# Performance work log

Measured on AMD Instinct MI355X. Metric: run time of the kernel, lower is better.

Reference implementation:

```python
import jax, jax.numpy as jnp
import numpy as np

HIDDEN = 128
RHO = 5        # K // 2 with K = 10
J = 5
SCALE = 5.0


def setup_inputs() -> dict:
    key = jax.random.key(0)
    ks = jax.random.split(key, 16)
    B, N, D = 2, 4096, HIDDEN
    eigvs = jax.random.uniform(ks[0], (B, N, D), dtype=jnp.float32)  # eigenvalue encodings in [0,1)
    x = jax.random.normal(ks[1], (B, N, D), dtype=jnp.float32)
    U = jax.random.normal(ks[2], (B, N, N), dtype=jnp.float32) / np.sqrt(N)
    s = 1.0 / np.sqrt(D)
    return {
        "eigvs": eigvs, "x": x, "U": U,
        # Linear weights stored as [in, out] (already transposed vs torch)
        "Wa": jax.random.normal(ks[3], (D, RHO), dtype=jnp.float32) * s,
        "ba": jnp.zeros((RHO,), jnp.float32),
        "Wb": jax.random.normal(ks[4], (D, RHO), dtype=jnp.float32) * s,
        "bb": jnp.zeros((RHO,), jnp.float32),
        "Ws": jax.random.normal(ks[5], (D, J), dtype=jnp.float32) * s,
        "bs": jnp.zeros((J,), jnp.float32),
        "WS": jax.random.normal(ks[6], (D, D), dtype=jnp.float32) * s,
        "bS": jnp.zeros((D,), jnp.float32),
        "WM": jax.random.normal(ks[7], (J, D, D), dtype=jnp.float32) * s,
        "bM": jnp.zeros((J, D), jnp.float32),
        "Ww": jax.random.normal(ks[8], (D, D), dtype=jnp.float32) * s,
        "bw": jnp.zeros((D,), jnp.float32),
    }


def _generate_g(a, sx, rho):
    # a: [B, rho]; sx: [B, J, N, D] scaled eigenvalues. Even Chebyshev polys.
    T_odd = jnp.ones_like(sx)
    T_even = sx
    g = a[:, 0, None, None, None] * T_even
    for i in range(1, rho):
        T_odd = 2.0 * sx * T_even - T_odd
        T_even = 2.0 * sx * T_odd - T_even
        g = g + a[:, i, None, None, None] * T_even
    return g


def _generate_h(b, e, rho):
    # b: [B, rho]; e: [B, N, D]. Odd Chebyshev polys.
    T_odd = jnp.ones_like(e)
    T_even = e
    h = b[:, 0, None, None] * T_odd
    for i in range(1, rho):
        T_odd = 2.0 * e * T_even - T_odd
        T_even = 2.0 * e * T_odd - T_even
        h = h + b[:, i, None, None] * T_odd
    return h


def reference(eigvs, x, U, Wa, ba, Wb, bb, Ws, bs, WS, bS, WM, bM, Ww, bw):
    # Filter coefficients from pooled eigenvalue encodings
    a_tilde = (eigvs @ Wa + ba).mean(axis=-2)                      # [B, rho]
    b_tilde = (eigvs @ Wb + bb).mean(axis=-2)                      # [B, rho]
    scale_tilde = jax.nn.sigmoid((eigvs @ Ws + bs).mean(axis=-2)) * SCALE  # [B, J]

    h = _generate_h(b_tilde, eigvs, RHO)                           # [B, N, D] scaling filter
    sx = scale_tilde[:, :, None, None] * eigvs[:, None]            # [B, J, N, D]
    g = _generate_g(a_tilde, sx, RHO)                              # [B, J, N, D] wavelet filters

    # Spectral convolution: U diag(filter) U^T x, per channel
    xt = jnp.einsum('bmn,bmd->bnd', U, x)                          # U^T x
    y_h = jnp.einsum('bnm,bmd->bnd', U, h * xt)                    # [B, N, D]
    y_g = jnp.einsum('bnm,bjmd->bjnd', U, g * xt[:, None])         # [B, J, N, D]

    out = y_h @ WS + bS                                            # S_kernel
    out = out + jnp.einsum('bjnd,jde->bne', y_g, WM) + bM.sum(0)   # sum_j M_kernels[j]
    return out @ Ww + bw                                           # W
```

## Files before the change

kernel.cpp:

```cpp
#include <hip/hip_runtime.h>
#include <hip/hip_bf16.h>
#include <stdint.h>

typedef unsigned short u16;
typedef __attribute__((ext_vector_type(8))) short bf16x8;
typedef __attribute__((ext_vector_type(4))) float f32x4;
typedef __attribute__((ext_vector_type(4))) uint32_t u32x4;

__device__ inline u16 f2bf(float f) {
  union { float f; uint32_t u; } v; v.f = f;
  uint32_t u = v.u;
  u += 0x7FFFu + ((u >> 16) & 1u);
  return (u16)(u >> 16);
}
__device__ inline uint32_t pkbf(float a, float b) {
  union { __hip_bfloat162 h; uint32_t u; } c;
  c.h = __float22bfloat162_rn(float2{a, b});
  return c.u;
}
__device__ inline float bf2f(u16 h) {
  union { uint32_t u; float f; } v; v.u = (uint32_t)h << 16; return v.f;
}
__device__ inline void gl_lds16(const void* g, void* s) {
  __builtin_amdgcn_global_load_lds(
      (const __attribute__((address_space(1))) void*)(uintptr_t)(g),
      (__attribute__((address_space(3))) void*)(uint32_t)(uintptr_t)(s),
      16, 0, 0);
}

__global__ __launch_bounds__(256) void k_pre(
    const float* __restrict__ eig, const float* __restrict__ x,
    const float* __restrict__ WS, const float* __restrict__ WM,
    const float* __restrict__ Ww, const float* __restrict__ bS,
    const float* __restrict__ bM, const float* __restrict__ bw,
    float* __restrict__ part, u16* __restrict__ xT,
    u16* __restrict__ VT, float* __restrict__ cvec) {
  const int bid = blockIdx.x, t = threadIdx.x;
  __shared__ float red[256];
  __shared__ uint32_t L[64][33];
  if (bid < 64) {
    const int b = bid >> 5, chunk = bid & 31;
    const int d = t & 127, half = t >> 7;
    const float* p = eig + ((long)b * 4096 + chunk * 128 + half) * 128 + d;
    float s = 0.0f;
    for (int i = 0; i < 64; i++) s += p[(long)i * 256];
    red[t] = s;
    __syncthreads();
    if (t < 128) part[((long)b * 32 + chunk) * 128 + d] = red[t] + red[t + 128];
    return;
  }
  if (bid < 320) {
    const int q = bid - 64;
    const int b = q >> 7, rem = q & 127;
    const int tr = rem & 63, tc = rem >> 6;
    const float* I = x + (long)b * 524288;
    u16* O = xT + (long)b * 524288;
    const int r = t >> 2, cq = (t & 3) * 4;
    const float* src = I + (long)(tr * 64 + r) * 128 + tc * 64;
#pragma unroll
    for (int i = 0; i < 4; i++) {
      const float4 f = *(const float4*)(src + cq + 16 * i);
      const int c = cq + 16 * i;
      L[r][(c >> 1)]     = pkbf(f.x, f.y);
      L[r][(c >> 1) + 1] = pkbf(f.z, f.w);
    }
    __syncthreads();
    const int r0 = (t & 7) * 8;
#pragma unroll
    for (int p = 0; p < 2; p++) {
      const int c = (t >> 3) + 32 * p;
      uint32_t w[4];
#pragma unroll
      for (int i = 0; i < 4; i++) {
        const uint32_t w0 = L[r0 + 2 * i][c >> 1];
        const uint32_t w1 = L[r0 + 2 * i + 1][c >> 1];
        const u16 v0 = (c & 1) ? (u16)(w0 >> 16) : (u16)(w0 & 0xffff);
        const u16 v1 = (c & 1) ? (u16)(w1 >> 16) : (u16)(w1 & 0xffff);
        w[i] = (uint32_t)v0 | ((uint32_t)v1 << 16);
      }
      u32x4* dst = (u32x4*)(O + (long)(tc * 64 + c) * 4096 + tr * 64 + r0);
      *dst = u32x4{w[0], w[1], w[2], w[3]};
    }
    return;
  }
  if (bid < 704) {
    const int q = (bid - 320) * 2 + (t >> 7);
    const int e = t & 127;
    const int f = q >> 7, d = q & 127;
    const float* Frow = (f == 0) ? (WS + d * 128) : (WM + ((long)(f - 1) * 128 + d) * 128);
    float s = 0.0f;
    for (int k = 0; k < 128; k++) s += Frow[k] * Ww[k * 128 + e];
    VT[(long)e * 768 + f * 128 + d] = f2bf(s);
    return;
  }
  if (t >= 128) return;
  float s = bw[t];
  for (int k = 0; k < 128; k++) {
    float tv = bS[k];
#pragma unroll
    for (int j = 0; j < 5; j++) tv += bM[j * 128 + k];
    s += tv * Ww[k * 128 + t];
  }
  cvec[t] = s;
}

__global__ __launch_bounds__(256) void k_gemm1(
    const u16* __restrict__ xT, const float* __restrict__ U,
    const float* __restrict__ part,
    const float* __restrict__ Wa, const float* __restrict__ ba,
    const float* __restrict__ Wb, const float* __restrict__ bb_,
    const float* __restrict__ Ws, const float* __restrict__ bs,
    float* __restrict__ xs, float* __restrict__ coeff) {
  const int tn = blockIdx.x, ks = blockIdx.y, bb = blockIdx.z;
  const int tid = threadIdx.x;
  __shared__ float sd[128];
  __shared__ __align__(16) u16 As[128 * 32];
  __shared__ __align__(16) u16 Bs[128 * 34 + 64];
  if (tn == 32) {
    if (ks != 0) return;
    if (tid < 128) {
      float s = 0.0f;
      for (int c = 0; c < 32; c++) s += part[((long)bb * 32 + c) * 128 + tid];
      sd[tid] = s * (1.0f / 4096.0f);
    }
    __syncthreads();
    if (tid >= 15) return;
    const int kind = tid / 5, r = tid % 5;
    const float* W = (kind == 0) ? Wa : ((kind == 1) ? Wb : Ws);
    float v = 0.0f;
    for (int d = 0; d < 128; d++) v += sd[d] * W[d * 5 + r];
    v += (kind == 0) ? ba[r] : ((kind == 1) ? bb_[r] : bs[r]);
    if (kind == 2) v = 5.0f / (1.0f + __expf(-v));
    coeff[bb * 16 + kind * 5 + r] = v;
    return;
  }
  const int wave = tid >> 6, lane = tid & 63;
  const int wm = (wave >> 1) * 64, wn = (wave & 1) * 64;
  f32x4 acc[4][4];
#pragma unroll
  for (int i = 0; i < 4; i++)
#pragma unroll
    for (int j = 0; j < 4; j++)
#pragma unroll
      for (int r = 0; r < 4; r++) acc[i][j][r] = 0.0f;
  const int a_off = (wm + (lane & 15)) * 64 + (lane >> 4) * 16;
  const int b_off = (wn + (lane & 15)) * 68 + (lane >> 4) * 16;
  const int srow = wave * 32 + (lane >> 2);
  const int scol = (lane & 3) * 8;
  const u16* Ab = xT + (long)bb * 524288 + ks * 512;
  const int q = tid & 15, cb = tid >> 4;
  const float* Bbase = U + (long)bb * 16777216 + tn * 128 + cb * 8;
  float4 ca0, ca1, cc0, cc1;
  {
    const float* r0 = Bbase + (long)(ks * 512 + 2 * q) * 4096;
    ca0 = *(const float4*)(r0); ca1 = *(const float4*)(r0 + 4);
    const float* r1 = r0 + 4096;
    cc0 = *(const float4*)(r1); cc1 = *(const float4*)(r1 + 4);
  }
  for (int k0 = 0; k0 < 512; k0 += 32) {
#pragma unroll
    for (int i = 0; i < 2; i++)
      gl_lds16(Ab + (long)(srow + i * 16) * 4096 + k0 + scol,
               (char*)As + (wave * 32 + i * 16) * 64);
    {
      uint32_t* dw = (uint32_t*)Bs;
      const int base = (cb * 8) * 17 + q;
      dw[base + 0 * 17] = pkbf(ca0.x, cc0.x);
      dw[base + 1 * 17] = pkbf(ca0.y, cc0.y);
      dw[base + 2 * 17] = pkbf(ca0.z, cc0.z);
      dw[base + 3 * 17] = pkbf(ca0.w, cc0.w);
      dw[base + 4 * 17] = pkbf(ca1.x, cc1.x);
      dw[base + 5 * 17] = pkbf(ca1.y, cc1.y);
      dw[base + 6 * 17] = pkbf(ca1.z, cc1.z);
      dw[base + 7 * 17] = pkbf(ca1.w, cc1.w);
    }
    __syncthreads();
    const int kn = (k0 + 32 < 512) ? (k0 + 32) : k0;
    float4 na0, na1, nc0, nc1;
    {
      const float* r0 = Bbase + (long)(ks * 512 + kn + 2 * q) * 4096;
      na0 = *(const float4*)(r0); na1 = *(const float4*)(r0 + 4);
      const float* r1 = r0 + 4096;
      nc0 = *(const float4*)(r1); nc1 = *(const float4*)(r1 + 4);
    }
    bf16x8 af[4], bfr[4];
#pragma unroll
    for (int mt = 0; mt < 4; mt++)
      af[mt] = *(const bf16x8*)((const char*)As + a_off + mt * 1024);
#pragma unroll
    for (int nt = 0; nt < 4; nt++)
      bfr[nt] = *(const bf16x8*)((const char*)Bs + b_off + nt * 1088);
#pragma unroll
    for (int mt = 0; mt < 4; mt++)
#pragma unroll
      for (int nt = 0; nt < 4; nt++)
        acc[mt][nt] = __builtin_amdgcn_mfma_f32_16x16x32_bf16(af[mt], bfr[nt], acc[mt][nt], 0, 0, 0);
    __syncthreads();
    ca0 = na0; ca1 = na1; cc0 = nc0; cc1 = nc1;
  }
  const int lr = (lane >> 4) * 4, lc = lane & 15;
  float* Cf = xs + (long)bb * 524288 + (long)ks * 1048576;
#pragma unroll
  for (int mt = 0; mt < 4; mt++)
#pragma unroll
    for (int nt = 0; nt < 4; nt++) {
      const int col = tn * 128 + wn + nt * 16 + lc;
#pragma unroll
      for (int r = 0; r < 4; r++) {
        const int row = wm + mt * 16 + lr + r;
        Cf[(long)col * 128 + row] = acc[mt][nt][r];
      }
    }
}

__global__ void k_filter(const float* __restrict__ eig, const float* __restrict__ xs,
                         const float* __restrict__ coeff, u16* __restrict__ Mod) {
  const int b = blockIdx.y;
  const int n = blockIdx.x * 2 + (threadIdx.x >> 7);
  const int d = threadIdx.x & 127;
  const long ridx = (long)b * 4096 + n;
  const long off = ridx * 128 + d;
  const float e = eig[off];
  float xv = 0.0f;
#pragma unroll
  for (int s = 0; s < 8; s++) xv += xs[off + (long)s * 1048576];
  const float* cf = coeff + b * 16;
  float To = 1.0f, Tev = e;
  float h = cf[5];
#pragma unroll
  for (int i = 1; i < 5; i++) {
    To = 2.0f * e * Tev - To;
    Tev = 2.0f * e * To - Tev;
    h += cf[5 + i] * To;
  }
  u16* row = Mod + ridx * 768;
  row[d] = f2bf(h * xv);
#pragma unroll
  for (int j = 0; j < 5; j++) {
    const float sx = cf[10 + j] * e;
    float To2 = 1.0f, Te2 = sx;
    float g = cf[0] * Te2;
#pragma unroll
    for (int i = 1; i < 5; i++) {
      To2 = 2.0f * sx * Te2 - To2;
      Te2 = 2.0f * sx * To2 - Te2;
      g += cf[i] * Te2;
    }
    row[(j + 1) * 128 + d] = f2bf(g * xv);
  }
}

__global__ __launch_bounds__(256) void k_gemm2(
    const u16* __restrict__ VT, const u16* __restrict__ Mod, u16* __restrict__ wT) {
  const int tn = blockIdx.x, bb = blockIdx.z;
  __shared__ __align__(16) u16 As[128 * 32];
  __shared__ __align__(16) u16 Bs[128 * 32];
  const int tid = threadIdx.x, wave = tid >> 6, lane = tid & 63;
  const int wm = (wave >> 1) * 64, wn = (wave & 1) * 64;
  f32x4 acc[4][4];
#pragma unroll
  for (int i = 0; i < 4; i++)
#pragma unroll
    for (int j = 0; j < 4; j++)
#pragma unroll
      for (int r = 0; r < 4; r++) acc[i][j][r] = 0.0f;
  const int a_off = (wm + (lane & 15)) * 64 + (lane >> 4) * 16;
  const int b_off = (wn + (lane & 15)) * 64 + (lane >> 4) * 16;
  const int srow = wave * 32 + (lane >> 2);
  const int scol = (lane & 3) * 8;
  const u16* Bb = Mod + (long)bb * 3145728 + (long)tn * 128 * 768;
  for (int k0 = 0; k0 < 768; k0 += 32) {
#pragma unroll
    for (int i = 0; i < 2; i++) {
      gl_lds16(VT + (long)(srow + i * 16) * 768 + k0 + scol,
               (char*)As + (wave * 32 + i * 16) * 64);
      gl_lds16(Bb + (long)(srow + i * 16) * 768 + k0 + scol,
               (char*)Bs + (wave * 32 + i * 16) * 64);
    }
    __syncthreads();
    bf16x8 af[4], bfr[4];
#pragma unroll
    for (int mt = 0; mt < 4; mt++)
      af[mt] = *(const bf16x8*)((const char*)As + a_off + mt * 1024);
#pragma unroll
    for (int nt = 0; nt < 4; nt++)
      bfr[nt] = *(const bf16x8*)((const char*)Bs + b_off + nt * 1024);
#pragma unroll
    for (int mt = 0; mt < 4; mt++)
#pragma unroll
      for (int nt = 0; nt < 4; nt++)
        acc[mt][nt] = __builtin_amdgcn_mfma_f32_16x16x32_bf16(af[mt], bfr[nt], acc[mt][nt], 0, 0, 0);
    __syncthreads();
  }
  const int lr = (lane >> 4) * 4, lc = lane & 15;
  u16* Cb = wT + (long)bb * 524288;
#pragma unroll
  for (int mt = 0; mt < 4; mt++)
#pragma unroll
    for (int nt = 0; nt < 4; nt++) {
      const int col = tn * 128 + wn + nt * 16 + lc;
#pragma unroll
      for (int r = 0; r < 4; r++) {
        const int row = wm + mt * 16 + lr + r;
        Cb[(long)row * 4096 + col] = f2bf(acc[mt][nt][r]);
      }
    }
}

__global__ __launch_bounds__(256) void k_gemm3(
    const float* __restrict__ U, const u16* __restrict__ wT, u16* __restrict__ os16) {
  const int tm = blockIdx.x, ks = blockIdx.y, bb = blockIdx.z;
  __shared__ __align__(16) u16 As[128 * 32];
  __shared__ __align__(16) u16 Bs[128 * 32];
  const int tid = threadIdx.x, wave = tid >> 6, lane = tid & 63;
  const int wm = (wave >> 1) * 64, wn = (wave & 1) * 64;
  f32x4 acc[4][4];
#pragma unroll
  for (int i = 0; i < 4; i++)
#pragma unroll
    for (int j = 0; j < 4; j++)
#pragma unroll
      for (int r = 0; r < 4; r++) acc[i][j][r] = 0.0f;
  const int a_off = (wm + (lane & 15)) * 64 + (lane >> 4) * 16;
  const int b_off = (wn + (lane & 15)) * 64 + (lane >> 4) * 16;
  const int srow = wave * 32 + (lane >> 2);
  const int scol = (lane & 3) * 8;
  const float* Abase = U + (long)bb * 16777216 +
                       (long)(tm * 128 + (tid >> 2)) * 4096 + (tid & 3) * 8;
  const u16* Bb = wT + (long)bb * 524288 + ks * 512;
  float4 cf0, cf1, cg0, cg1;
  {
    const float* s0 = Abase + ks * 512;
    cf0 = *(const float4*)(s0); cf1 = *(const float4*)(s0 + 4);
    const float* s1 = s0 + 262144;
    cg0 = *(const float4*)(s1); cg1 = *(const float4*)(s1 + 4);
  }
  for (int k0 = 0; k0 < 512; k0 += 32) {
#pragma unroll
    for (int i = 0; i < 2; i++)
      gl_lds16(Bb + (long)(srow + i * 16) * 4096 + k0 + scol,
               (char*)Bs + (wave * 32 + i * 16) * 64);
    *(u32x4*)((char*)As + tid * 16) =
        u32x4{pkbf(cf0.x, cf0.y), pkbf(cf0.z, cf0.w), pkbf(cf1.x, cf1.y), pkbf(cf1.z, cf1.w)};
    *(u32x4*)((char*)As + 4096 + tid * 16) =
        u32x4{pkbf(cg0.x, cg0.y), pkbf(cg0.z, cg0.w), pkbf(cg1.x, cg1.y), pkbf(cg1.z, cg1.w)};
    __syncthreads();
    const int kn = (k0 + 32 < 512) ? (k0 + 32) : k0;
    float4 nf0, nf1, ng0, ng1;
    {
      const float* s0 = Abase + ks * 512 + kn;
      nf0 = *(const float4*)(s0); nf1 = *(const float4*)(s0 + 4);
      const float* s1 = s0 + 262144;
      ng0 = *(const float4*)(s1); ng1 = *(const float4*)(s1 + 4);
    }
    bf16x8 af[4], bfr[4];
#pragma unroll
    for (int mt = 0; mt < 4; mt++)
      af[mt] = *(const bf16x8*)((const char*)As + a_off + mt * 1024);
#pragma unroll
    for (int nt = 0; nt < 4; nt++)
      bfr[nt] = *(const bf16x8*)((const char*)Bs + b_off + nt * 1024);
#pragma unroll
    for (int mt = 0; mt < 4; mt++)
#pragma unroll
      for (int nt = 0; nt < 4; nt++)
        acc[mt][nt] = __builtin_amdgcn_mfma_f32_16x16x32_bf16(af[mt], bfr[nt], acc[mt][nt], 0, 0, 0);
    __syncthreads();
    cf0 = nf0; cf1 = nf1; cg0 = ng0; cg1 = ng1;
  }
  const int lr = (lane >> 4) * 4, lc = lane & 15;
  u16* Cb = os16 + (long)ks * 1048576 + (long)bb * 524288;
#pragma unroll
  for (int mt = 0; mt < 4; mt++)
#pragma unroll
    for (int nt = 0; nt < 4; nt++) {
      const int col = wn + nt * 16 + lc;
#pragma unroll
      for (int r = 0; r < 4; r++) {
        const int row = tm * 128 + wm + mt * 16 + lr + r;
        Cb[(long)row * 128 + col] = f2bf(acc[mt][nt][r]);
      }
    }
}

__global__ void k_outred(const u16* __restrict__ os16, const float* __restrict__ cvec,
                         float* __restrict__ out) {
  const long i = (long)blockIdx.x * 256 + threadIdx.x;
  const long j4 = i * 4;
  float4 r = {0.0f, 0.0f, 0.0f, 0.0f};
#pragma unroll
  for (int s = 0; s < 8; s++) {
    const uint2 v = *(const uint2*)(os16 + j4 + (long)s * 1048576);
    r.x += bf2f((u16)(v.x & 0xffff));
    r.y += bf2f((u16)(v.x >> 16));
    r.z += bf2f((u16)(v.y & 0xffff));
    r.w += bf2f((u16)(v.y >> 16));
  }
  const float4 cv = *(const float4*)(cvec + (i & 31) * 4);
  r.x += cv.x; r.y += cv.y; r.z += cv.z; r.w += cv.w;
  *(float4*)(out + j4) = r;
}

extern "C" void kernel_launch(void* const* d_in, const int* in_sizes, int n_in,
                              void* d_out, int out_size, void* d_ws, size_t ws_size,
                              hipStream_t stream) {
  const float* eig = (const float*)d_in[0];
  const float* x   = (const float*)d_in[1];
  const float* U   = (const float*)d_in[2];
  const float* Wa  = (const float*)d_in[3];
  const float* ba  = (const float*)d_in[4];
  const float* Wb  = (const float*)d_in[5];
  const float* bb  = (const float*)d_in[6];
  const float* Ws  = (const float*)d_in[7];
  const float* bs  = (const float*)d_in[8];
  const float* WSm = (const float*)d_in[9];
  const float* bS  = (const float*)d_in[10];
  const float* WM  = (const float*)d_in[11];
  const float* bM  = (const float*)d_in[12];
  const float* Ww  = (const float*)d_in[13];
  const float* bw  = (const float*)d_in[14];

  char* ws = (char*)d_ws;
  float* xs   = (float*)(ws + 0);
  u16*   os16 = (u16*)(ws + 0);
  u16*   Mod  = (u16*)(ws + 33554432);
  u16*   xT   = (u16*)(ws + 46137344);
  u16*   wT   = (u16*)(ws + 48234496);
  u16*   VT   = (u16*)(ws + 50331648);
  float* part = (float*)(ws + 50528256);
  float* coef = (float*)(ws + 50561024);
  float* cvec = (float*)(ws + 50561152);
  float* outp = (float*)d_out;

  if (ws_size < (size_t)50561664) return;

  k_pre<<<705, 256, 0, stream>>>(eig, x, WSm, WM, Ww, bS, bM, bw, part, xT, VT, cvec);

  k_gemm1<<<dim3(33, 8, 2), 256, 0, stream>>>(xT, U, part, Wa, ba, Wb, bb, Ws, bs, xs, coef);

  k_filter<<<dim3(2048, 2), 256, 0, stream>>>(eig, xs, coef, Mod);

  k_gemm2<<<dim3(32, 1, 2), 256, 0, stream>>>(VT, Mod, wT);

  k_gemm3<<<dim3(32, 8, 2), 256, 0, stream>>>(U, wT, os16);

  k_outred<<<1024, 256, 0, stream>>>(os16, cvec, outp);
}
```

Before: 293.9 us.

## Store gemm1 split-K partials in bf16 and atomically reduce gemm3 into output

The split-K partials of the first GEMM are now written in bf16 rather than fp32, which halves the traffic k_filter reads. The separate k_outred kernel is removed. k_pre now fills the output with the bias vector, and k_gemm3 adds its split-K partials straight into the output with float atomics. This drops one launch and the os16 round trip, at the cost of atomic contention, nondeterministic summation order and extra bf16 rounding in xs.

```diff
diff --git a/kernel.cpp b/kernel.cpp
--- a/kernel.cpp
+++ b/kernel.cpp
@@ -34,7 +34,7 @@
     const float* __restrict__ Ww, const float* __restrict__ bS,
     const float* __restrict__ bM, const float* __restrict__ bw,
     float* __restrict__ part, u16* __restrict__ xT,
-    u16* __restrict__ VT, float* __restrict__ cvec) {
+    u16* __restrict__ VT, float* __restrict__ outp) {
   const int bid = blockIdx.x, t = threadIdx.x;
   __shared__ float red[256];
   __shared__ uint32_t L[64][33];
@@ -93,15 +93,29 @@
     VT[(long)e * 768 + f * 128 + d] = f2bf(s);
     return;
   }
-  if (t >= 128) return;
-  float s = bw[t];
-  for (int k = 0; k < 128; k++) {
-    float tv = bS[k];
-#pragma unroll
-    for (int j = 0; j < 5; j++) tv += bM[j * 128 + k];
-    s += tv * Ww[k * 128 + t];
-  }
-  cvec[t] = s;
+  {
+    const int q2 = bid - 704;
+    __shared__ float cv[128];
+    if (t < 128) {
+      float s = bw[t];
+      for (int k = 0; k < 128; k++) {
+        float tv = bS[k];
+#pragma unroll
+        for (int j = 0; j < 5; j++) tv += bM[j * 128 + k];
+        s += tv * Ww[k * 128 + t];
+      }
+      cv[t] = s;
+    }
+    __syncthreads();
+    float* O = outp + (long)q2 * 16384;
+#pragma unroll
+    for (int i = 0; i < 16; i++) {
+      const int idx4 = i * 256 + t;
+      const int e0 = (idx4 * 4) & 127;
+      float4 v = {cv[e0], cv[e0 + 1], cv[e0 + 2], cv[e0 + 3]};
+      *(float4*)(O + (long)idx4 * 4) = v;
+    }
+  }
 }
 
 __global__ __launch_bounds__(256) void k_gemm1(
@@ -110,7 +124,7 @@
     const float* __restrict__ Wa, const float* __restrict__ ba,
     const float* __restrict__ Wb, const float* __restrict__ bb_,
     const float* __restrict__ Ws, const float* __restrict__ bs,
-    float* __restrict__ xs, float* __restrict__ coeff) {
+    u16* __restrict__ xs16, float* __restrict__ coeff) {
   const int tn = blockIdx.x, ks = blockIdx.y, bb = blockIdx.z;
   const int tid = threadIdx.x;
   __shared__ float sd[128];
@@ -199,7 +213,7 @@
     ca0 = na0; ca1 = na1; cc0 = nc0; cc1 = nc1;
   }
   const int lr = (lane >> 4) * 4, lc = lane & 15;
-  float* Cf = xs + (long)bb * 524288 + (long)ks * 1048576;
+  u16* Cf = xs16 + (long)ks * 1048576 + (long)bb * 524288;
 #pragma unroll
   for (int mt = 0; mt < 4; mt++)
 #pragma unroll
@@ -208,12 +222,12 @@
 #pragma unroll
       for (int r = 0; r < 4; r++) {
         const int row = wm + mt * 16 + lr + r;
-        Cf[(long)col * 128 + row] = acc[mt][nt][r];
+        Cf[(long)col * 128 + row] = f2bf(acc[mt][nt][r]);
       }
     }
 }
 
-__global__ void k_filter(const float* __restrict__ eig, const float* __restrict__ xs,
+__global__ void k_filter(const float* __restrict__ eig, const u16* __restrict__ xs16,
                          const float* __restrict__ coeff, u16* __restrict__ Mod) {
   const int b = blockIdx.y;
   const int n = blockIdx.x * 2 + (threadIdx.x >> 7);
@@ -223,7 +237,7 @@
   const float e = eig[off];
   float xv = 0.0f;
 #pragma unroll
-  for (int s = 0; s < 8; s++) xv += xs[off + (long)s * 1048576];
+  for (int s = 0; s < 8; s++) xv += bf2f(xs16[off + (long)s * 1048576]);
   const float* cf = coeff + b * 16;
   float To = 1.0f, Tev = e;
   float h = cf[5];
@@ -308,7 +322,7 @@
 }
 
 __global__ __launch_bounds__(256) void k_gemm3(
-    const float* __restrict__ U, const u16* __restrict__ wT, u16* __restrict__ os16) {
+    const float* __restrict__ U, const u16* __restrict__ wT, float* __restrict__ outp) {
   const int tm = blockIdx.x, ks = blockIdx.y, bb = blockIdx.z;
   __shared__ __align__(16) u16 As[128 * 32];
   __shared__ __align__(16) u16 Bs[128 * 32];
@@ -369,7 +383,7 @@
     cf0 = nf0; cf1 = nf1; cg0 = ng0; cg1 = ng1;
   }
   const int lr = (lane >> 4) * 4, lc = lane & 15;
-  u16* Cb = os16 + (long)ks * 1048576 + (long)bb * 524288;
+  float* Co = outp + (long)bb * 524288;
 #pragma unroll
   for (int mt = 0; mt < 4; mt++)
 #pragma unroll
@@ -378,27 +392,9 @@
 #pragma unroll
       for (int r = 0; r < 4; r++) {
         const int row = tm * 128 + wm + mt * 16 + lr + r;
-        Cb[(long)row * 128 + col] = f2bf(acc[mt][nt][r]);
+        unsafeAtomicAdd(Co + (long)row * 128 + col, acc[mt][nt][r]);
       }
     }
-}
-
-__global__ void k_outred(const u16* __restrict__ os16, const float* __restrict__ cvec,
-                         float* __restrict__ out) {
-  const long i = (long)blockIdx.x * 256 + threadIdx.x;
-  const long j4 = i * 4;
-  float4 r = {0.0f, 0.0f, 0.0f, 0.0f};
-#pragma unroll
-  for (int s = 0; s < 8; s++) {
-    const uint2 v = *(const uint2*)(os16 + j4 + (long)s * 1048576);
-    r.x += bf2f((u16)(v.x & 0xffff));
-    r.y += bf2f((u16)(v.x >> 16));
-    r.z += bf2f((u16)(v.y & 0xffff));
-    r.w += bf2f((u16)(v.y >> 16));
-  }
-  const float4 cv = *(const float4*)(cvec + (i & 31) * 4);
-  r.x += cv.x; r.y += cv.y; r.z += cv.z; r.w += cv.w;
-  *(float4*)(out + j4) = r;
 }
 
 extern "C" void kernel_launch(void* const* d_in, const int* in_sizes, int n_in,
@@ -421,28 +417,24 @@
   const float* bw  = (const float*)d_in[14];
 
   char* ws = (char*)d_ws;
-  float* xs   = (float*)(ws + 0);
-  u16*   os16 = (u16*)(ws + 0);
-  u16*   Mod  = (u16*)(ws + 33554432);
-  u16*   xT   = (u16*)(ws + 46137344);
-  u16*   wT   = (u16*)(ws + 48234496);
-  u16*   VT   = (u16*)(ws + 50331648);
-  float* part = (float*)(ws + 50528256);
-  float* coef = (float*)(ws + 50561024);
-  float* cvec = (float*)(ws + 50561152);
+  u16*   xs16 = (u16*)(ws + 0);
+  u16*   Mod  = (u16*)(ws + 16777216);
+  u16*   xT   = (u16*)(ws + 29360128);
+  u16*   wT   = (u16*)(ws + 31457280);
+  u16*   VT   = (u16*)(ws + 33554432);
+  float* part = (float*)(ws + 33751040);
+  float* coef = (float*)(ws + 33783808);
   float* outp = (float*)d_out;
 
-  if (ws_size < (size_t)50561664) return;
-
-  k_pre<<<705, 256, 0, stream>>>(eig, x, WSm, WM, Ww, bS, bM, bw, part, xT, VT, cvec);
-
-  k_gemm1<<<dim3(33, 8, 2), 256, 0, stream>>>(xT, U, part, Wa, ba, Wb, bb, Ws, bs, xs, coef);
-
-  k_filter<<<dim3(2048, 2), 256, 0, stream>>>(eig, xs, coef, Mod);
+  if (ws_size < (size_t)33784064) return;
+
+  k_pre<<<768, 256, 0, stream>>>(eig, x, WSm, WM, Ww, bS, bM, bw, part, xT, VT, outp);
+
+  k_gemm1<<<dim3(33, 8, 2), 256, 0, stream>>>(xT, U, part, Wa, ba, Wb, bb, Ws, bs, xs16, coef);
+
+  k_filter<<<dim3(2048, 2), 256, 0, stream>>>(eig, xs16, coef, Mod);
 
   k_gemm2<<<dim3(32, 1, 2), 256, 0, stream>>>(VT, Mod, wT);
 
-  k_gemm3<<<dim3(32, 8, 2), 256, 0, stream>>>(U, wT, os16);
-
-  k_outred<<<1024, 256, 0, stream>>>(os16, cvec, outp);
-}
+  k_gemm3<<<dim3(32, 8, 2), 256, 0, stream>>>(U, wT, outp);
+}
```

New measurement: 305.8 us. 1.04x slower.
